# Kernel tuning notes

Measured on AMD Instinct MI355X. Metric: run time of the kernel, lower is better.

The kernel has to match this reference:

```python
import jax, jax.numpy as jnp
import numpy as np

B, S, H = 1, 2048, 2048
NH, KVH, D = 32, 8, 64
G = NH // KVH  # num_key_value_groups = 4


def setup_inputs() -> dict:
    key = jax.random.key(0)
    k1, k2, k3 = jax.random.split(key, 3)
    x = jax.random.normal(k1, (B, S, H), dtype=jnp.float32)
    w_qkv = jax.random.normal(k2, ((NH + 2 * KVH) * D, H), dtype=jnp.float32) * 0.02
    w_o = jax.random.normal(k3, (H, NH * D), dtype=jnp.float32) * 0.02
    return {"x": x, "w_qkv": w_qkv, "w_o": w_o}


def _rope_cos_sin(seqlen, dim, dtype):
    inv_freq = 1.0 / (10000.0 ** (jnp.arange(0, dim, 2, dtype=jnp.float32) / dim))
    t = jnp.arange(seqlen, dtype=jnp.float32)
    freqs = jnp.outer(t, inv_freq)  # [S, D/2]
    return jnp.cos(freqs).astype(dtype), jnp.sin(freqs).astype(dtype)


def _apply_rope(x, cos, sin):
    # x: [B,S,h,D]; non-interleaved half rotation (flash-attn RotaryEmbedding)
    d2 = x.shape[-1] // 2
    x1, x2 = x[..., :d2], x[..., d2:]
    c = cos[None, :, None, :]
    s = sin[None, :, None, :]
    return jnp.concatenate([x1 * c - x2 * s, x2 * c + x1 * s], axis=-1)


def reference(x, w_qkv, w_o):
    b, s, _ = x.shape
    qkv = x @ w_qkv.T  # fused QKV proj: [B,S,(NH+2*KVH)*D]
    q, kv = jnp.split(qkv, [NH * D], axis=-1)
    q = q.reshape(b, s, NH, D)
    kv = kv.reshape(b, s, 2, KVH, D)
    cos, sin = _rope_cos_sin(s, D, x.dtype)
    q = _apply_rope(q, cos, sin)
    k = _apply_rope(kv[:, :, 0], cos, sin)
    v = kv[:, :, 1]
    # GQA: group q heads per kv head instead of repeat_interleave (same math)
    qg = q.reshape(b, s, KVH, G, D)
    scale = 1.0 / np.sqrt(D).astype(np.float32)
    scores = jnp.einsum('bskgd,btkd->bkgst', qg, k) * scale  # [B,KVH,G,S,S]
    causal = jnp.tril(jnp.ones((s, s), dtype=bool))
    scores = jnp.where(causal[None, None, None], scores, jnp.asarray(-jnp.inf, scores.dtype))
    p = jax.nn.softmax(scores, axis=-1)
    out = jnp.einsum('bkgst,btkd->bskgd', p, v).reshape(b, s, NH * D)
    return out @ w_o.T
```

## Files before the change

### kernel.cpp

```cpp
#include <hip/hip_runtime.h>


typedef __bf16 bf16_t;
typedef __attribute__((ext_vector_type(8))) __bf16 bf16x8;
typedef __attribute__((ext_vector_type(4))) __bf16 bf16x4;
typedef __attribute__((ext_vector_type(4))) float f32x4;
typedef __attribute__((ext_vector_type(2))) unsigned int u32x2;
typedef __attribute__((ext_vector_type(4))) unsigned int u32x4;

#define S_LEN 2048
#define H_DIM 2048
#define NHEAD 32
#define KVH 8
#define HD 64
#define QKV_N 3072

#define NE_PER_KH 288
#define NSPLIT_PER_KH 280
#define ENT_BYTES 16896

__global__ void cast3_kernel(const float* __restrict__ x, const float* __restrict__ wq,
                             const float* __restrict__ wo, bf16_t* __restrict__ xb,
                             bf16_t* __restrict__ wqb, bf16_t* __restrict__ wob) {
  int i = blockIdx.x * blockDim.x + threadIdx.x;
  const int n1 = S_LEN * H_DIM / 4, n2 = QKV_N * H_DIM / 4, n3 = H_DIM * H_DIM / 4;
  const float* src; bf16_t* dst; int j;
  if (i < n1)           { src = x;  dst = xb;  j = i; }
  else if (i < n1 + n2) { src = wq; dst = wqb; j = i - n1; }
  else if (i < n1 + n2 + n3) { src = wo; dst = wob; j = i - n1 - n2; }
  else return;
  float4 v = ((const float4*)src)[j];
  bf16x4 o;
  o.x = (bf16_t)v.x; o.y = (bf16_t)v.y; o.z = (bf16_t)v.z; o.w = (bf16_t)v.w;
  ((bf16x4*)dst)[j] = o;
}

__device__ __forceinline__ void async_copy16(bf16_t* lds_base, const bf16_t* g) {
  __builtin_amdgcn_global_load_lds(
      (const __attribute__((address_space(1))) unsigned int*)g,
      (__attribute__((address_space(3))) unsigned int*)lds_base, 16, 0, 0);
}

#define GBM 128
#define GBN 128

template <int EPI>
__global__ __launch_bounds__(512, 4) void gemm_sk(const bf16_t* __restrict__ A,
                                                  const bf16_t* __restrict__ B,
                                                  float* __restrict__ C,
                                                  bf16_t* __restrict__ qb,
                                                  bf16_t* __restrict__ ktp,
                                                  bf16_t* __restrict__ vt2,
                                                  int M, int N, int K) {
  __shared__ __align__(16) bf16_t As[2][GBM * 64];
  __shared__ __align__(16) bf16_t Bs[2][GBM * 64];

  const int tid  = threadIdx.x;
  const int lane = tid & 63;
  const int w    = tid >> 6;
  const int wq   = w & 3;
  const int gw   = w >> 2;
  const int wm   = (wq >> 1) * 64;
  const int wn   = (wq & 1) * 64;
  const int c    = lane & 15;
  const int quad = lane >> 4;
  const int m0   = blockIdx.y * GBM;
  const int n0   = blockIdx.x * GBN;

  f32x4 acc[4][4] = {};

  const bf16_t* Ab = A + (size_t)m0 * K;
  const bf16_t* Bb = B + (size_t)n0 * K;

  int srow[2], skc[2], sb[2];
#pragma unroll
  for (int i = 0; i < 2; ++i) {
    int p = i * 512 + tid;
    srow[i] = p >> 3;
    skc[i]  = (p & 7) ^ (srow[i] & 7);
    sb[i]   = (i * 512 + w * 64) * 8;
  }

  auto stage = [&](int buf, int k0) {
#pragma unroll
    for (int i = 0; i < 2; ++i) {
      async_copy16(&As[buf][sb[i]], Ab + (size_t)srow[i] * K + k0 + skc[i] * 8);
      async_copy16(&Bs[buf][sb[i]], Bb + (size_t)srow[i] * K + k0 + skc[i] * 8);
    }
  };

  auto compute = [&](int buf) {
    bf16x8 af[4], bfr[4];
#pragma unroll
    for (int mt = 0; mt < 4; ++mt) {
      int row = wm + mt * 16 + c;
      af[mt] = *(const bf16x8*)&As[buf][(row * 8 + ((gw * 4 + quad) ^ (row & 7))) * 8];
    }
#pragma unroll
    for (int nt = 0; nt < 4; ++nt) {
      int rowb = wn + nt * 16 + c;
      bfr[nt] = *(const bf16x8*)&Bs[buf][(rowb * 8 + ((gw * 4 + quad) ^ (rowb & 7))) * 8];
    }
#pragma unroll
    for (int mt = 0; mt < 4; ++mt)
#pragma unroll
      for (int nt = 0; nt < 4; ++nt)
        acc[mt][nt] = __builtin_amdgcn_mfma_f32_16x16x32_bf16(af[mt], bfr[nt], acc[mt][nt], 0, 0, 0);
  };

  const int NI = K >> 6;
  stage(0, 0);
  int buf = 0;
  for (int it = 0; it < NI; ++it) {
    asm volatile("s_waitcnt vmcnt(0)" ::: "memory");
    __builtin_amdgcn_s_barrier();
    if (it + 1 < NI) stage(buf ^ 1, (it + 1) << 6);
    compute(buf);
    buf ^= 1;
  }

  __syncthreads();
  float* xch = (float*)&As[0][0];
  if (gw == 1) {
#pragma unroll
    for (int t16 = 0; t16 < 16; ++t16)
      *(f32x4*)&xch[wq * 4096 + (t16 * 64 + lane) * 4] = acc[t16 >> 2][t16 & 3];
  }
  __syncthreads();
  if (gw == 0) {
#pragma unroll
    for (int t16 = 0; t16 < 16; ++t16) {
      f32x4 o = *(const f32x4*)&xch[wq * 4096 + (t16 * 64 + lane) * 4];
      acc[t16 >> 2][t16 & 3] += o;
    }

    if (EPI == 0) {
#pragma unroll
      for (int mt = 0; mt < 4; ++mt)
#pragma unroll
        for (int nt = 0; nt < 4; ++nt)
#pragma unroll
          for (int reg = 0; reg < 4; ++reg) {
            int row = m0 + wm + mt * 16 + quad * 4 + reg;
            int col = n0 + wn + nt * 16 + c;
            C[(size_t)row * N + col] = acc[mt][nt][reg];
          }
    } else {
      const int colb = n0 + wn;
      if (colb < NHEAD * HD) {
        const int h = colb >> 6;
#pragma unroll
        for (int nt = 0; nt < 2; ++nt) {
          const int i = nt * 16 + c;
          const float invf = __expf(-(float)i * (9.210340371976184f / 32.0f));
#pragma unroll
          for (int mt = 0; mt < 4; ++mt)
#pragma unroll
            for (int reg = 0; reg < 4; ++reg) {
              const int s = m0 + wm + mt * 16 + quad * 4 + reg;
              float sn, cs;
              __sincosf((float)s * invf, &sn, &cs);
              const float x1 = acc[mt][nt][reg], x2 = acc[mt][nt + 2][reg];
              bf16_t* q = qb + (size_t)s * H_DIM + h * HD;
              q[i]      = (bf16_t)((x1 * cs - x2 * sn) * 0.125f);
              q[i + 32] = (bf16_t)((x2 * cs + x1 * sn) * 0.125f);
            }
        }
      } else if (colb < NHEAD * HD + KVH * HD) {
        const int kh = (colb - NHEAD * HD) >> 6;
#pragma unroll
        for (int nt = 0; nt < 2; ++nt) {
          const int i = nt * 16 + c;
          const float invf = __expf(-(float)i * (9.210340371976184f / 32.0f));
#pragma unroll
          for (int mt = 0; mt < 4; ++mt)
#pragma unroll
            for (int reg = 0; reg < 4; ++reg) {
              const int s = m0 + wm + mt * 16 + quad * 4 + reg;
              float sn, cs;
              __sincosf((float)s * invf, &sn, &cs);
              const float x1 = acc[mt][nt][reg], x2 = acc[mt][nt + 2][reg];
              bf16_t* kd = ktp + ((size_t)kh * S_LEN + s) * HD;
              kd[i]      = (bf16_t)(x1 * cs - x2 * sn);
              kd[i + 32] = (bf16_t)(x2 * cs + x1 * sn);
            }
        }
      } else {
        const int kh = (colb - NHEAD * HD - KVH * HD) >> 6;
#pragma unroll
        for (int nt = 0; nt < 4; ++nt) {
          const int d = nt * 16 + c;
#pragma unroll
          for (int mt = 0; mt < 4; ++mt) {
            const int sr = m0 + wm + mt * 16 + quad * 4;
            bf16x4 pv;
#pragma unroll
            for (int reg = 0; reg < 4; ++reg) pv[reg] = (bf16_t)acc[mt][nt][reg];
            *(bf16x4*)&vt2[((size_t)kh * HD + d) * S_LEN + sr] = pv;
          }
        }
      }
    }
  }
}

__global__ __launch_bounds__(256, 4) void flash_split(const bf16_t* __restrict__ qb,
                                                      const bf16_t* __restrict__ kt,
                                                      const bf16_t* __restrict__ vt2,
                                                      float* __restrict__ pbuf,
                                                      bf16_t* __restrict__ attn) {
  __shared__ __align__(16) bf16_t Ks[2][64 * 64];
  __shared__ __align__(16) bf16_t Vs[2][64 * 64];

  const int tid  = threadIdx.x;
  const int lane = tid & 63;
  const int w    = tid >> 6;
  const int e    = (int)gridDim.x - 1 - (int)blockIdx.x;
  const int kh   = e / NE_PER_KH;
  const int j    = e - kh * NE_PER_KH;

  int qt, chunk, nch;
  if (j < 8) {
    qt = j; chunk = 0; nch = 1;
  } else {
    int j2 = j - 8;
    qt = 8;
    for (;;) {
      int Tq = (qt >> 1) + 1;
      nch = (Tq + 3) >> 2;
      if (j2 < nch) { chunk = j2; break; }
      j2 -= nch; ++qt;
    }
  }
  const int T       = (qt >> 1) + 1;
  const int t_begin = (chunk * T) / nch;
  const int t_end   = ((chunk + 1) * T) / nch;

  const int s0    = qt * 32;
  const int h     = kh * 4 + w;
  const int c     = lane & 15;
  const int quad  = lane >> 4;

  const int idx0 = (c + (quad & 1) * 32) * 4;
  const int idx1 = idx0 + 64;
  const bool hiY = quad >= 2;

  bf16x8 qf[2][2];
#pragma unroll
  for (int rf = 0; rf < 2; ++rf)
#pragma unroll
    for (int ks = 0; ks < 2; ++ks)
      qf[rf][ks] = *(const bf16x8*)(qb + (size_t)(s0 + rf * 16 + c) * H_DIM + h * HD + ks * 32 + quad * 8);

  f32x4 acc[2][4] = {};
  float lsum[2] = {0.f, 0.f};

  const bf16_t* kbase = kt + (size_t)kh * S_LEN * HD;
  const bf16_t* vbase = vt2 + (size_t)kh * HD * S_LEN;

  int srow[2], skc[2], sbase[2];
#pragma unroll
  for (int i2 = 0; i2 < 2; ++i2) {
    int chunkbase = i2 * 256 + w * 64;
    int p = chunkbase + lane;
    sbase[i2] = chunkbase * 8;
    srow[i2]  = p >> 3;
    skc[i2]   = (p & 7) ^ (srow[i2] & 7);
  }

  auto stage = [&](int buf, int tile) {
    const int t0 = tile * 64;
#pragma unroll
    for (int i2 = 0; i2 < 2; ++i2) {
      async_copy16(&Ks[buf][sbase[i2]], kbase + (size_t)(t0 + srow[i2]) * HD + skc[i2] * 8);
      async_copy16(&Vs[buf][sbase[i2]], vbase + (size_t)srow[i2] * S_LEN + t0 + skc[i2] * 8);
    }
  };

  stage(0, t_begin);
  int buf = 0;
  for (int tile = t_begin; tile < t_end; ++tile) {
    const int t0 = tile * 64;
    asm volatile("s_waitcnt vmcnt(0)" ::: "memory");
    __builtin_amdgcn_s_barrier();
    if (tile + 1 < t_end) stage(buf ^ 1, tile + 1);

    const bool masked = (tile == T - 1);

#pragma unroll
    for (int kh2 = 0; kh2 < 2; ++kh2) {
      unsigned pw[2][2][2];
#pragma unroll
      for (int kt2l = 0; kt2l < 2; ++kt2l) {
        const int kt2 = kh2 * 2 + kt2l;
        bf16x8 kf0 = *(const bf16x8*)&Ks[buf][((kt2 * 16 + c) * 8 + ((quad) ^ (c & 7))) * 8];
        bf16x8 kf1 = *(const bf16x8*)&Ks[buf][((kt2 * 16 + c) * 8 + ((4 + quad) ^ (c & 7))) * 8];
#pragma unroll
        for (int rf = 0; rf < 2; ++rf) {
          f32x4 st = {};
          __builtin_amdgcn_s_setprio(1);
          st = __builtin_amdgcn_mfma_f32_16x16x32_bf16(kf0, qf[rf][0], st, 0, 0, 0);
          st = __builtin_amdgcn_mfma_f32_16x16x32_bf16(kf1, qf[rf][1], st, 0, 0, 0);
          __builtin_amdgcn_s_setprio(0);
          const int row = s0 + rf * 16 + c;
          bf16x4 pk;
#pragma unroll
          for (int reg = 0; reg < 4; ++reg) {
            const int key = t0 + kt2 * 16 + quad * 4 + reg;
            float p = __expf(st[reg] - 8.0f);
            if (masked && key > row) p = 0.f;
            pk[reg] = (bf16_t)p;
            lsum[rf] += p;
          }
          u32x2 pv2 = __builtin_bit_cast(u32x2, pk);
          pw[rf][kt2l][0] = pv2.x;
          pw[rf][kt2l][1] = pv2.y;
        }
      }

      bf16x8 vf[4];
#pragma unroll
      for (int dt = 0; dt < 4; ++dt)
        vf[dt] = *(const bf16x8*)&Vs[buf][((dt * 16 + c) * 8 + ((kh2 * 4 + quad) ^ (c & 7))) * 8];

#pragma unroll
      for (int rf = 0; rf < 2; ++rf) {
        int lo, hi;
        u32x4 fwv;
        lo = __builtin_amdgcn_ds_bpermute(idx0, (int)pw[rf][0][0]);
        hi = __builtin_amdgcn_ds_bpermute(idx0, (int)pw[rf][1][0]);
        fwv.x = hiY ? (unsigned)hi : (unsigned)lo;
        lo = __builtin_amdgcn_ds_bpermute(idx0, (int)pw[rf][0][1]);
        hi = __builtin_amdgcn_ds_bpermute(idx0, (int)pw[rf][1][1]);
        fwv.y = hiY ? (unsigned)hi : (unsigned)lo;
        lo = __builtin_amdgcn_ds_bpermute(idx1, (int)pw[rf][0][0]);
        hi = __builtin_amdgcn_ds_bpermute(idx1, (int)pw[rf][1][0]);
        fwv.z = hiY ? (unsigned)hi : (unsigned)lo;
        lo = __builtin_amdgcn_ds_bpermute(idx1, (int)pw[rf][0][1]);
        hi = __builtin_amdgcn_ds_bpermute(idx1, (int)pw[rf][1][1]);
        fwv.w = hiY ? (unsigned)hi : (unsigned)lo;
        bf16x8 pa = __builtin_bit_cast(bf16x8, fwv);
        __builtin_amdgcn_s_setprio(1);
#pragma unroll
        for (int dt = 0; dt < 4; ++dt)
          acc[rf][dt] = __builtin_amdgcn_mfma_f32_16x16x32_bf16(pa, vf[dt], acc[rf][dt], 0, 0, 0);
        __builtin_amdgcn_s_setprio(0);
      }
    }
    buf ^= 1;
  }

#pragma unroll
  for (int rf = 0; rf < 2; ++rf) {
    lsum[rf] += __shfl_xor(lsum[rf], 16);
    lsum[rf] += __shfl_xor(lsum[rf], 32);
  }

  __syncthreads();
  if (j < 8) {
    float* lbuf = (float*)&Ks[0][0] + w * 32;
#pragma unroll
    for (int rf = 0; rf < 2; ++rf) lbuf[rf * 16 + c] = lsum[rf];
    asm volatile("s_waitcnt lgkmcnt(0)" ::: "memory");
#pragma unroll
    for (int rf = 0; rf < 2; ++rf)
#pragma unroll
      for (int reg = 0; reg < 4; ++reg) {
        const float inv = 1.0f / lbuf[rf * 16 + quad * 4 + reg];
        const int row = s0 + rf * 16 + quad * 4 + reg;
#pragma unroll
        for (int dt = 0; dt < 4; ++dt)
          attn[(size_t)row * H_DIM + h * HD + dt * 16 + c] = (bf16_t)(acc[rf][dt][reg] * inv);
      }
  } else {
    const int slot = kh * NSPLIT_PER_KH + (j - 8);
    char* ent = (char*)pbuf + (size_t)slot * ENT_BYTES;
    bf16_t* eo = (bf16_t*)ent;
    float*  el = (float*)(ent + 16384);
#pragma unroll
    for (int rf = 0; rf < 2; ++rf) {
#pragma unroll
      for (int dt = 0; dt < 4; ++dt)
#pragma unroll
        for (int reg = 0; reg < 4; ++reg)
          eo[w * 2048 + (rf * 16 + quad * 4 + reg) * 64 + dt * 16 + c] = (bf16_t)acc[rf][dt][reg];
      el[w * 32 + rf * 16 + c] = lsum[rf];
    }
  }
}

__global__ __launch_bounds__(256) void flash_reduce(const float* __restrict__ pbuf,
                                                    bf16_t* __restrict__ attn) {
  const int kh = blockIdx.x / 56;
  const int qt = 8 + (blockIdx.x % 56);

  int base = 0;
  for (int q = 8; q < qt; ++q) {
    int Tq = (q >> 1) + 1;
    base += (Tq + 3) >> 2;
  }
  const int T   = (qt >> 1) + 1;
  const int nch = (T + 3) >> 2;
  base += kh * NSPLIT_PER_KH;

  const int t   = threadIdx.x;
  const int h2  = t >> 6;
  const int row = (t >> 1) & 31;
  const int dh  = t & 1;

  f32x4 o[8] = {};
  float l = 0.f;
  for (int ci = 0; ci < nch; ++ci) {
    const char* ent = (const char*)pbuf + (size_t)(base + ci) * ENT_BYTES;
    const bf16_t* p = (const bf16_t*)ent + h2 * 2048 + row * 64 + dh * 32;
#pragma unroll
    for (int jj = 0; jj < 8; ++jj) {
      bf16x4 v = ((const bf16x4*)p)[jj];
      o[jj][0] += (float)v[0]; o[jj][1] += (float)v[1];
      o[jj][2] += (float)v[2]; o[jj][3] += (float)v[3];
    }
    l += ((const float*)(ent + 16384))[h2 * 32 + row];
  }
  const float inv = 1.0f / l;
  bf16_t* dst = attn + (size_t)(qt * 32 + row) * H_DIM + (kh * 4 + h2) * 64 + dh * 32;
#pragma unroll
  for (int jj = 0; jj < 8; ++jj) {
    bf16x4 ov;
    ov[0] = (bf16_t)(o[jj][0] * inv); ov[1] = (bf16_t)(o[jj][1] * inv);
    ov[2] = (bf16_t)(o[jj][2] * inv); ov[3] = (bf16_t)(o[jj][3] * inv);
    *(bf16x4*)(dst + jj * 4) = ov;
  }
}

extern "C" void kernel_launch(void* const* d_in, const int* in_sizes, int n_in,
                              void* d_out, int out_size, void* d_ws, size_t ws_size,
                              hipStream_t stream) {
  const float* x     = (const float*)d_in[0];
  const float* w_qkv = (const float*)d_in[1];
  const float* w_o   = (const float*)d_in[2];
  float* out = (float*)d_out;

  char* ws = (char*)d_ws;
  const size_t OVERLAY = (size_t)1280 * 8320 * 4;
  bf16_t* x_bf    = (bf16_t*)ws;
  bf16_t* wqkv_bf = (bf16_t*)(ws + (size_t)S_LEN * H_DIM * 2);
  float*  pbuf    = (float*)ws;
  size_t off = OVERLAY;
  bf16_t* wo_bf   = (bf16_t*)(ws + off); off += (size_t)H_DIM * H_DIM * 2;
  bf16_t* q_bf    = (bf16_t*)(ws + off); off += (size_t)S_LEN * H_DIM * 2;
  bf16_t* k_t     = (bf16_t*)(ws + off); off += (size_t)KVH * S_LEN * HD * 2;
  bf16_t* v_t2    = (bf16_t*)(ws + off); off += (size_t)KVH * S_LEN * HD * 2;
  bf16_t* attn    = (bf16_t*)(ws + off); off += (size_t)S_LEN * H_DIM * 2;

  const int ntot = (S_LEN * H_DIM + QKV_N * H_DIM + H_DIM * H_DIM) / 4;
  cast3_kernel<<<(ntot + 255) / 256, 256, 0, stream>>>(x, w_qkv, w_o, x_bf, wqkv_bf, wo_bf);

  gemm_sk<1><<<dim3(QKV_N / GBN, S_LEN / GBM), 512, 0, stream>>>(
      x_bf, wqkv_bf, nullptr, q_bf, k_t, v_t2, S_LEN, QKV_N, H_DIM);

  flash_split<<<8 * NE_PER_KH, 256, 0, stream>>>(q_bf, k_t, v_t2, pbuf, attn);
  flash_reduce<<<8 * 56, 256, 0, stream>>>(pbuf, attn);

  gemm_sk<0><<<dim3(H_DIM / GBN, S_LEN / GBM), 512, 0, stream>>>(
      attn, wo_bf, out, nullptr, nullptr, nullptr, S_LEN, H_DIM, H_DIM);
}
```

Baseline: 214.5 us.

## Shrink flash key tiles to 32 to cut causal waste and raise occupancy

```diff
diff --git a/kernel.cpp b/kernel.cpp
--- a/kernel.cpp
+++ b/kernel.cpp
@@ -204,13 +204,13 @@
   }
 }
 
-__global__ __launch_bounds__(256, 4) void flash_split(const bf16_t* __restrict__ qb,
+__global__ __launch_bounds__(256, 6) void flash_split(const bf16_t* __restrict__ qb,
                                                       const bf16_t* __restrict__ kt,
                                                       const bf16_t* __restrict__ vt2,
                                                       float* __restrict__ pbuf,
                                                       bf16_t* __restrict__ attn) {
-  __shared__ __align__(16) bf16_t Ks[2][64 * 64];
-  __shared__ __align__(16) bf16_t Vs[2][64 * 64];
+  __shared__ __align__(16) bf16_t Ks[2][32 * 64];
+  __shared__ __align__(16) bf16_t Vs[2][64 * 32];
 
   const int tid  = threadIdx.x;
   const int lane = tid & 63;
@@ -226,13 +226,12 @@
     int j2 = j - 8;
     qt = 8;
     for (;;) {
-      int Tq = (qt >> 1) + 1;
-      nch = (Tq + 3) >> 2;
+      nch = (qt + 8) >> 3;
       if (j2 < nch) { chunk = j2; break; }
       j2 -= nch; ++qt;
     }
   }
-  const int T       = (qt >> 1) + 1;
+  const int T       = qt + 1;
   const int t_begin = (chunk * T) / nch;
   const int t_end   = ((chunk + 1) * T) / nch;
 
@@ -258,94 +257,83 @@
   const bf16_t* kbase = kt + (size_t)kh * S_LEN * HD;
   const bf16_t* vbase = vt2 + (size_t)kh * HD * S_LEN;
 
-  int srow[2], skc[2], sbase[2];
-#pragma unroll
-  for (int i2 = 0; i2 < 2; ++i2) {
-    int chunkbase = i2 * 256 + w * 64;
-    int p = chunkbase + lane;
-    sbase[i2] = chunkbase * 8;
-    srow[i2]  = p >> 3;
-    skc[i2]   = (p & 7) ^ (srow[i2] & 7);
-  }
+  const int krow = tid >> 3;
+  const int kkc  = (tid & 7) ^ (krow & 7);
+  const int vrow = tid >> 2;
+  const int vkc  = (tid & 3) ^ (vrow & 3);
+  const int sbase = w * 64 * 8;
 
   auto stage = [&](int buf, int tile) {
-    const int t0 = tile * 64;
-#pragma unroll
-    for (int i2 = 0; i2 < 2; ++i2) {
-      async_copy16(&Ks[buf][sbase[i2]], kbase + (size_t)(t0 + srow[i2]) * HD + skc[i2] * 8);
-      async_copy16(&Vs[buf][sbase[i2]], vbase + (size_t)srow[i2] * S_LEN + t0 + skc[i2] * 8);
-    }
+    const int t0 = tile * 32;
+    async_copy16(&Ks[buf][sbase], kbase + (size_t)(t0 + krow) * HD + kkc * 8);
+    async_copy16(&Vs[buf][sbase], vbase + (size_t)vrow * S_LEN + t0 + vkc * 8);
   };
 
   stage(0, t_begin);
   int buf = 0;
   for (int tile = t_begin; tile < t_end; ++tile) {
-    const int t0 = tile * 64;
+    const int t0 = tile * 32;
     asm volatile("s_waitcnt vmcnt(0)" ::: "memory");
     __builtin_amdgcn_s_barrier();
     if (tile + 1 < t_end) stage(buf ^ 1, tile + 1);
 
     const bool masked = (tile == T - 1);
 
-#pragma unroll
-    for (int kh2 = 0; kh2 < 2; ++kh2) {
-      unsigned pw[2][2][2];
-#pragma unroll
-      for (int kt2l = 0; kt2l < 2; ++kt2l) {
-        const int kt2 = kh2 * 2 + kt2l;
-        bf16x8 kf0 = *(const bf16x8*)&Ks[buf][((kt2 * 16 + c) * 8 + ((quad) ^ (c & 7))) * 8];
-        bf16x8 kf1 = *(const bf16x8*)&Ks[buf][((kt2 * 16 + c) * 8 + ((4 + quad) ^ (c & 7))) * 8];
-#pragma unroll
-        for (int rf = 0; rf < 2; ++rf) {
-          f32x4 st = {};
-          __builtin_amdgcn_s_setprio(1);
-          st = __builtin_amdgcn_mfma_f32_16x16x32_bf16(kf0, qf[rf][0], st, 0, 0, 0);
-          st = __builtin_amdgcn_mfma_f32_16x16x32_bf16(kf1, qf[rf][1], st, 0, 0, 0);
-          __builtin_amdgcn_s_setprio(0);
-          const int row = s0 + rf * 16 + c;
-          bf16x4 pk;
-#pragma unroll
-          for (int reg = 0; reg < 4; ++reg) {
-            const int key = t0 + kt2 * 16 + quad * 4 + reg;
-            float p = __expf(st[reg] - 8.0f);
-            if (masked && key > row) p = 0.f;
-            pk[reg] = (bf16_t)p;
-            lsum[rf] += p;
-          }
-          u32x2 pv2 = __builtin_bit_cast(u32x2, pk);
-          pw[rf][kt2l][0] = pv2.x;
-          pw[rf][kt2l][1] = pv2.y;
+    unsigned pw[2][2][2];
+#pragma unroll
+    for (int kt2 = 0; kt2 < 2; ++kt2) {
+      bf16x8 kf0 = *(const bf16x8*)&Ks[buf][((kt2 * 16 + c) * 8 + ((quad) ^ (c & 7))) * 8];
+      bf16x8 kf1 = *(const bf16x8*)&Ks[buf][((kt2 * 16 + c) * 8 + ((4 + quad) ^ (c & 7))) * 8];
+#pragma unroll
+      for (int rf = 0; rf < 2; ++rf) {
+        f32x4 st = {};
+        __builtin_amdgcn_s_setprio(1);
+        st = __builtin_amdgcn_mfma_f32_16x16x32_bf16(kf0, qf[rf][0], st, 0, 0, 0);
+        st = __builtin_amdgcn_mfma_f32_16x16x32_bf16(kf1, qf[rf][1], st, 0, 0, 0);
+        __builtin_amdgcn_s_setprio(0);
+        const int row = s0 + rf * 16 + c;
+        bf16x4 pk;
+#pragma unroll
+        for (int reg = 0; reg < 4; ++reg) {
+          const int key = t0 + kt2 * 16 + quad * 4 + reg;
+          float p = __builtin_amdgcn_exp2f(fmaf(st[reg], 1.44269504f, -11.54156036f));
+          if (masked && key > row) p = 0.f;
+          pk[reg] = (bf16_t)p;
+          lsum[rf] += p;
         }
+        u32x2 pv2 = __builtin_bit_cast(u32x2, pk);
+        pw[rf][kt2][0] = pv2.x;
+        pw[rf][kt2][1] = pv2.y;
       }
-
-      bf16x8 vf[4];
+    }
+
+    bf16x8 vf[4];
+#pragma unroll
+    for (int dt = 0; dt < 4; ++dt)
+      vf[dt] = *(const bf16x8*)&Vs[buf][((dt * 16 + c) * 4 + (quad ^ (c & 3))) * 8];
+
+#pragma unroll
+    for (int rf = 0; rf < 2; ++rf) {
+      int lo, hi;
+      u32x4 fwv;
+      lo = __builtin_amdgcn_ds_bpermute(idx0, (int)pw[rf][0][0]);
+      hi = __builtin_amdgcn_ds_bpermute(idx0, (int)pw[rf][1][0]);
+      fwv.x = hiY ? (unsigned)hi : (unsigned)lo;
+      lo = __builtin_amdgcn_ds_bpermute(idx0, (int)pw[rf][0][1]);
+      hi = __builtin_amdgcn_ds_bpermute(idx0, (int)pw[rf][1][1]);
+      fwv.y = hiY ? (unsigned)hi : (unsigned)lo;
+      lo = __builtin_amdgcn_ds_bpermute(idx1, (int)pw[rf][0][0]);
+      hi = __builtin_amdgcn_ds_bpermute(idx1, (int)pw[rf][1][0]);
+      fwv.z = hiY ? (unsigned)hi : (unsigned)lo;
+      lo = __builtin_amdgcn_ds_bpermute(idx1, (int)pw[rf][0][1]);
+      hi = __builtin_amdgcn_ds_bpermute(idx1, (int)pw[rf][1][1]);
+      fwv.w = hiY ? (unsigned)hi : (unsigned)lo;
+      bf16x8 pa = __builtin_bit_cast(bf16x8, fwv);
+      __builtin_amdgcn_s_setprio(1);
 #pragma unroll
       for (int dt = 0; dt < 4; ++dt)
-        vf[dt] = *(const bf16x8*)&Vs[buf][((dt * 16 + c) * 8 + ((kh2 * 4 + quad) ^ (c & 7))) * 8];
-
-#pragma unroll
-      for (int rf = 0; rf < 2; ++rf) {
-        int lo, hi;
-        u32x4 fwv;
-        lo = __builtin_amdgcn_ds_bpermute(idx0, (int)pw[rf][0][0]);
-        hi = __builtin_amdgcn_ds_bpermute(idx0, (int)pw[rf][1][0]);
-        fwv.x = hiY ? (unsigned)hi : (unsigned)lo;
-        lo = __builtin_amdgcn_ds_bpermute(idx0, (int)pw[rf][0][1]);
-        hi = __builtin_amdgcn_ds_bpermute(idx0, (int)pw[rf][1][1]);
-        fwv.y = hiY ? (unsigned)hi : (unsigned)lo;
-        lo = __builtin_amdgcn_ds_bpermute(idx1, (int)pw[rf][0][0]);
-        hi = __builtin_amdgcn_ds_bpermute(idx1, (int)pw[rf][1][0]);
-        fwv.z = hiY ? (unsigned)hi : (unsigned)lo;
-        lo = __builtin_amdgcn_ds_bpermute(idx1, (int)pw[rf][0][1]);
-        hi = __builtin_amdgcn_ds_bpermute(idx1, (int)pw[rf][1][1]);
-        fwv.w = hiY ? (unsigned)hi : (unsigned)lo;
-        bf16x8 pa = __builtin_bit_cast(bf16x8, fwv);
-        __builtin_amdgcn_s_setprio(1);
-#pragma unroll
-        for (int dt = 0; dt < 4; ++dt)
-          acc[rf][dt] = __builtin_amdgcn_mfma_f32_16x16x32_bf16(pa, vf[dt], acc[rf][dt], 0, 0, 0);
-        __builtin_amdgcn_s_setprio(0);
-      }
+        acc[rf][dt] = __builtin_amdgcn_mfma_f32_16x16x32_bf16(pa, vf[dt], acc[rf][dt], 0, 0, 0);
+      __builtin_amdgcn_s_setprio(0);
     }
     buf ^= 1;
   }
@@ -395,12 +383,8 @@
   const int qt = 8 + (blockIdx.x % 56);
 
   int base = 0;
-  for (int q = 8; q < qt; ++q) {
-    int Tq = (q >> 1) + 1;
-    base += (Tq + 3) >> 2;
-  }
-  const int T   = (qt >> 1) + 1;
-  const int nch = (T + 3) >> 2;
+  for (int q = 8; q < qt; ++q) base += (q + 8) >> 3;
+  const int nch = (qt + 8) >> 3;
   base += kh * NSPLIT_PER_KH;
 
   const int t   = threadIdx.x;
```

Measured after the change: 277.0 us. 1.29x slower.
